# Optimization experiments

Measured on AMD Instinct MI355X. Metric: run time of the kernel, lower is better.

The kernel has to match this reference:

```python
import jax, jax.numpy as jnp
import numpy as np

B, T, F, U = 128, 512, 128, 512  # batch, time, features, GRU units


def _gru(x, W, Urec, bi, br, return_sequences):
    """Keras GRU (reset_after=True, recurrent_activation=sigmoid, activation=relu).
    x: (B, T, F_in); W: (F_in, 3U); Urec: (U, 3U); bi, br: (3U,). Gate order: z, r, h.
    """
    b = x.shape[0]
    u = Urec.shape[0]
    # precompute all input-projected gates: (T, B, 3U)
    gx = jnp.transpose(jnp.einsum('bti,ig->btg', x, W) + bi, (1, 0, 2))
    h0 = jnp.zeros((b, u), x.dtype)

    def step(h, g):
        rec = h @ Urec + br                      # (B, 3U)
        xz, xr, xh = jnp.split(g, 3, axis=-1)
        rz, rr, rh = jnp.split(rec, 3, axis=-1)
        z = jax.nn.sigmoid(xz + rz)              # update gate
        r = jax.nn.sigmoid(xr + rr)              # reset gate
        hh = jax.nn.relu(xh + r * rh)            # candidate (relu activation)
        h_new = z * h + (1.0 - z) * hh
        return h_new, h_new

    h_last, hs = jax.lax.scan(step, h0, gx)
    if return_sequences:
        return jnp.transpose(hs, (1, 0, 2))      # (B, T, U)
    return h_last                                # (B, U)


def setup_inputs() -> dict:
    key = jax.random.key(0)
    ks = jax.random.split(key, 8)
    s_in1 = 1.0 / np.sqrt(F)
    s_rec = 1.0 / np.sqrt(U)
    return {
        'x':   jax.random.normal(ks[0], (B, T, F), jnp.float32),
        'W1':  jax.random.normal(ks[1], (F, 3 * U), jnp.float32) * s_in1,
        'U1':  jax.random.normal(ks[2], (U, 3 * U), jnp.float32) * s_rec,
        'bi1': jnp.zeros((3 * U,), jnp.float32),
        'br1': jnp.zeros((3 * U,), jnp.float32),
        'W2':  jax.random.normal(ks[3], (U, 3 * U), jnp.float32) * s_rec,
        'U2':  jax.random.normal(ks[4], (U, 3 * U), jnp.float32) * s_rec,
        'bi2': jnp.zeros((3 * U,), jnp.float32),
        'br2': jnp.zeros((3 * U,), jnp.float32),
        'Wd':  jax.random.normal(ks[5], (U, 1), jnp.float32) * s_rec,
        'bd':  jnp.zeros((1,), jnp.float32),
    }


def reference(x, W1, U1, bi1, br1, W2, U2, bi2, br2, Wd, bd):
    h_seq = _gru(x, W1, U1, bi1, br1, True)      # (B, T, U)
    h = _gru(h_seq, W2, U2, bi2, br2, False)     # (B, U)
    return h @ Wd + bd
```

## Files before the change

### kernel.cpp

```cpp
#include <hip/hip_runtime.h>
#include <cstdint>
#include <cstddef>

#define B_  128
#define T_  512
#define F_  128
#define U_  512
#define G3  1536
#define BU  (B_ * U_)

#define NGRP 8
#define MB   16
#define GN   32
#define UC   16

typedef __attribute__((ext_vector_type(8))) _Float16 half8;
typedef __attribute__((ext_vector_type(4))) float    f32x4;

union HU16 { _Float16 h; unsigned short us; };

__device__ __forceinline__ float sigmoidf_(float x) {
    return 1.0f / (1.0f + __expf(-x));
}

__device__ __forceinline__ void vm_drain() {
    asm volatile("s_waitcnt vmcnt(0)" ::: "memory");
}

__device__ __forceinline__ void load_h16(const _Float16* aptr, half8* f) {
    asm volatile(
        "global_load_dwordx4 %0, %16, off offset:0 sc0 sc1\n\t"
        "global_load_dwordx4 %1, %16, off offset:64 sc0 sc1\n\t"
        "global_load_dwordx4 %2, %16, off offset:128 sc0 sc1\n\t"
        "global_load_dwordx4 %3, %16, off offset:192 sc0 sc1\n\t"
        "global_load_dwordx4 %4, %16, off offset:256 sc0 sc1\n\t"
        "global_load_dwordx4 %5, %16, off offset:320 sc0 sc1\n\t"
        "global_load_dwordx4 %6, %16, off offset:384 sc0 sc1\n\t"
        "global_load_dwordx4 %7, %16, off offset:448 sc0 sc1\n\t"
        "global_load_dwordx4 %8, %16, off offset:512 sc0 sc1\n\t"
        "global_load_dwordx4 %9, %16, off offset:576 sc0 sc1\n\t"
        "global_load_dwordx4 %10, %16, off offset:640 sc0 sc1\n\t"
        "global_load_dwordx4 %11, %16, off offset:704 sc0 sc1\n\t"
        "global_load_dwordx4 %12, %16, off offset:768 sc0 sc1\n\t"
        "global_load_dwordx4 %13, %16, off offset:832 sc0 sc1\n\t"
        "global_load_dwordx4 %14, %16, off offset:896 sc0 sc1\n\t"
        "global_load_dwordx4 %15, %16, off offset:960 sc0 sc1"
        : "=&v"(f[0]), "=&v"(f[1]), "=&v"(f[2]), "=&v"(f[3]),
          "=&v"(f[4]), "=&v"(f[5]), "=&v"(f[6]), "=&v"(f[7]),
          "=&v"(f[8]), "=&v"(f[9]), "=&v"(f[10]), "=&v"(f[11]),
          "=&v"(f[12]), "=&v"(f[13]), "=&v"(f[14]), "=&v"(f[15])
        : "v"((uint64_t)(uintptr_t)aptr)
        : "memory");
}

__device__ __forceinline__ void wait_h16(half8* f) {
    asm volatile(
        "s_waitcnt vmcnt(0)"
        : "+v"(f[0]), "+v"(f[1]), "+v"(f[2]), "+v"(f[3]),
          "+v"(f[4]), "+v"(f[5]), "+v"(f[6]), "+v"(f[7]),
          "+v"(f[8]), "+v"(f[9]), "+v"(f[10]), "+v"(f[11]),
          "+v"(f[12]), "+v"(f[13]), "+v"(f[14]), "+v"(f[15])
        :
        : "memory");
}

__device__ __forceinline__ void store_h4(_Float16* addr, unsigned v0, unsigned v1,
                                         unsigned v2, unsigned v3) {
    asm volatile(
        "global_store_short %0, %1, off sc0 sc1\n\t"
        "global_store_short %0, %2, off offset:1024 sc0 sc1\n\t"
        "global_store_short %0, %3, off offset:2048 sc0 sc1\n\t"
        "global_store_short %0, %4, off offset:3072 sc0 sc1"
        :: "v"((uint64_t)(uintptr_t)addr), "v"(v0), "v"(v1), "v"(v2), "v"(v3)
        : "memory");
}

__device__ __forceinline__ void flag_set(unsigned* p, unsigned val) {
    asm volatile("global_store_dword %0, %1, off sc0 sc1"
                 :: "v"((uint64_t)(uintptr_t)p), "v"(val) : "memory");
}

__device__ __forceinline__ unsigned flag_get(const unsigned* p) {
    unsigned v;
    asm volatile("global_load_dword %0, %1, off sc0 sc1\n\ts_waitcnt vmcnt(0)"
                 : "=v"(v) : "v"((uint64_t)(uintptr_t)p) : "memory");
    return v;
}

__device__ __forceinline__ void poll_flags(const unsigned* base, int lane, unsigned tgt) {
    const unsigned* p = base + (lane & 31);
    while (!__all((int)(flag_get(p) >= tgt))) {}
}

__global__ void cast_init_kernel(const float* __restrict__ x,
                                 _Float16* __restrict__ xh,
                                 _Float16* __restrict__ h1pub,
                                 _Float16* __restrict__ h2pub,
                                 unsigned int* __restrict__ gbar) {
    size_t i      = (size_t)blockIdx.x * blockDim.x + threadIdx.x;
    size_t stride = (size_t)gridDim.x * blockDim.x;
    for (size_t idx = i; idx < (size_t)B_ * T_ * F_; idx += stride)
        xh[idx] = (_Float16)x[idx];
    for (size_t idx = i; idx < (size_t)3 * BU; idx += stride)
        h1pub[idx] = (_Float16)0.f;
    for (size_t idx = i; idx < (size_t)2 * BU; idx += stride)
        h2pub[idx] = (_Float16)0.f;
    if (blockIdx.x == 0)
        for (int idx = threadIdx.x; idx < 2048; idx += blockDim.x)
            gbar[idx] = 0u;
}

__global__ void transpose_cast_kernel(const float* __restrict__ in,
                                      _Float16* __restrict__ out, int K) {
    __shared__ float tile[32][33];
    int n0 = blockIdx.x * 32;
    int k0 = blockIdx.y * 32;
    int tx = threadIdx.x, ty = threadIdx.y;
#pragma unroll
    for (int i = 0; i < 4; ++i)
        tile[ty + i * 8][tx] = in[(size_t)(k0 + ty + i * 8) * G3 + (n0 + tx)];
    __syncthreads();
#pragma unroll
    for (int i = 0; i < 4; ++i)
        out[(size_t)(n0 + ty + i * 8) * K + (k0 + tx)] =
            (_Float16)tile[tx][ty + i * 8];
}

__global__ __launch_bounds__(256) void gemm_gx1_kernel(
    const _Float16* __restrict__ xh,
    const _Float16* __restrict__ w1t,
    _Float16* __restrict__ gx1) {
    int bx = blockIdx.x;
    int mb = bx / 12, nb = bx % 12;
    int wave = threadIdx.x >> 6, lane = threadIdx.x & 63;
    int wm = wave >> 1, wn = wave & 1;
    int am = lane & 15, aq = lane >> 4;

    half8 af[2][4];
#pragma unroll
    for (int mt = 0; mt < 2; ++mt) {
        int mo = mb * 64 + wm * 32 + mt * 16 + am;
        int b = mo & 127, t = mo >> 7;
        const _Float16* ap = xh + ((size_t)b * T_ + t) * F_ + aq * 8;
#pragma unroll
        for (int kc = 0; kc < 4; ++kc)
            af[mt][kc] = *(const half8*)(ap + kc * 32);
    }

#pragma unroll
    for (int nt = 0; nt < 4; ++nt) {
        int n0 = nb * 128 + wn * 64 + nt * 16;
        f32x4 acc0 = {0.f, 0.f, 0.f, 0.f};
        f32x4 acc1 = {0.f, 0.f, 0.f, 0.f};
#pragma unroll
        for (int kc = 0; kc < 4; ++kc) {
            half8 bf = *(const half8*)(w1t + (size_t)(n0 + am) * F_ + kc * 32 + aq * 8);
            acc0 = __builtin_amdgcn_mfma_f32_16x16x32_f16(af[0][kc], bf, acc0, 0, 0, 0);
            acc1 = __builtin_amdgcn_mfma_f32_16x16x32_f16(af[1][kc], bf, acc1, 0, 0, 0);
        }
        int col = lane & 15, rb = (lane >> 4) * 4;
        int mbase0 = mb * 64 + wm * 32 + 0 * 16;
        int mbase1 = mb * 64 + wm * 32 + 1 * 16;
#pragma unroll
        for (int i = 0; i < 4; ++i) {
            gx1[(size_t)(mbase0 + rb + i) * G3 + n0 + col] = (_Float16)acc0[i];
            gx1[(size_t)(mbase1 + rb + i) * G3 + n0 + col] = (_Float16)acc1[i];
        }
    }
}

__global__ __launch_bounds__(192, 1) void gru_persist_kernel(
    const _Float16* __restrict__ gx1,
    const _Float16* __restrict__ u1t,
    const _Float16* __restrict__ w2t,
    const _Float16* __restrict__ u2t,
    const float* __restrict__ bi1, const float* __restrict__ br1,
    const float* __restrict__ bi2, const float* __restrict__ br2,
    _Float16* __restrict__ h1pub,
    _Float16* __restrict__ h2pub,
    float* __restrict__ h2fin,
    unsigned int* __restrict__ gbar) {
    __shared__ float scr[2 * 3 * 16 * 17];

    const int tid  = threadIdx.x;
    const int bx   = blockIdx.x;
    const int grp  = bx & 7;
    const int jj   = bx >> 3;
    const int wave = tid >> 6, lane = tid & 63;
    const int row0 = grp * MB;
    const int u0   = jj * UC;

    unsigned* flag1 = gbar + 512  + (size_t)grp * 32;
    unsigned* flag2 = gbar + 1024 + (size_t)grp * 32;
    unsigned* myflag1 = flag1 + jj;
    unsigned* myflag2 = flag2 + jj;

    const int col = lane & 15;
    const int rb4 = (lane >> 4) * 4;
    const int aq  = lane >> 4;
    const size_t a_elem = (size_t)(row0 + col) * U_ + aq * 8;
    const int u = u0 + col;

    const _Float16* wsrc = (wave == 0) ? u1t : (wave == 1) ? w2t : u2t;
    half8 bfr[3][16];
#pragma unroll
    for (int g = 0; g < 3; ++g)
#pragma unroll
        for (int kc = 0; kc < 16; ++kc)
            bfr[g][kc] = *(const half8*)(
                wsrc + (size_t)(g * U_ + u0 + col) * U_ + kc * 32 + aq * 8);

    float zb = 0.f, rb_ = 0.f, hbi = 0.f, hbr = 0.f;
    _Float16 pgz[4], pgr[4], pgh[4];
    if (wave == 0) {
        zb  = bi1[u] + br1[u];
        rb_ = bi1[U_ + u] + br1[U_ + u];
        hbi = bi1[2 * U_ + u];
        hbr = br1[2 * U_ + u];
        const _Float16* g0 = gx1 + ((size_t)0 * B_ + row0 + rb4) * G3;
#pragma unroll
        for (int i = 0; i < 4; ++i) {
            pgz[i] = g0[(size_t)i * G3 + u];
            pgr[i] = g0[(size_t)i * G3 + U_ + u];
            pgh[i] = g0[(size_t)i * G3 + 2 * U_ + u];
        }
    } else if (wave == 2) {
        zb  = bi2[u] + br2[u];
        rb_ = bi2[U_ + u] + br2[U_ + u];
        hbi = bi2[2 * U_ + u];
        hbr = br2[2 * U_ + u];
    }

    float st[4] = {0.f, 0.f, 0.f, 0.f};

    int wr3 = 0, rd3 = 2;
    for (int r = 0; r <= T_ + 1; ++r) {
        if (wave == 0) {
            if (r < T_) {
                poll_flags(flag1, lane, (unsigned)r);
                _Float16 ngz[4], ngr[4], ngh[4];
                bool pf = (r + 1 < T_);
                if (pf) {
                    const _Float16* g = gx1 + ((size_t)(r + 1) * B_ + row0 + rb4) * G3;
#pragma unroll
                    for (int i = 0; i < 4; ++i) {
                        ngz[i] = g[(size_t)i * G3 + u];
                        ngr[i] = g[(size_t)i * G3 + U_ + u];
                        ngh[i] = g[(size_t)i * G3 + 2 * U_ + u];
                    }
                }
                half8 f[16];
                load_h16(h1pub + (size_t)rd3 * BU + a_elem, f);
                wait_h16(f);
                f32x4 a0 = {0.f, 0.f, 0.f, 0.f};
                f32x4 a1 = {0.f, 0.f, 0.f, 0.f};
                f32x4 a2 = {0.f, 0.f, 0.f, 0.f};
#pragma unroll
                for (int kc = 0; kc < 16; ++kc) {
                    a0 = __builtin_amdgcn_mfma_f32_16x16x32_f16(f[kc], bfr[0][kc], a0, 0, 0, 0);
                    a1 = __builtin_amdgcn_mfma_f32_16x16x32_f16(f[kc], bfr[1][kc], a1, 0, 0, 0);
                    a2 = __builtin_amdgcn_mfma_f32_16x16x32_f16(f[kc], bfr[2][kc], a2, 0, 0, 0);
                }
                unsigned pv[4];
#pragma unroll
                for (int i = 0; i < 4; ++i) {
                    float z  = sigmoidf_((float)pgz[i] + a0[i] + zb);
                    float rg = sigmoidf_((float)pgr[i] + a1[i] + rb_);
                    float hh = fmaxf(0.f, (float)pgh[i] + hbi + rg * (a2[i] + hbr));
                    st[i] = z * st[i] + (1.f - z) * hh;
                    HU16 c; c.h = (_Float16)st[i]; pv[i] = c.us;
                }
                _Float16* dst = h1pub + (size_t)wr3 * BU +
                                (size_t)(row0 + rb4) * U_ + u;
                store_h4(dst, pv[0], pv[1], pv[2], pv[3]);
                vm_drain();
                if (lane == 0) flag_set(myflag1, (unsigned)(r + 1));
                if (pf) {
#pragma unroll
                    for (int i = 0; i < 4; ++i) {
                        pgz[i] = ngz[i]; pgr[i] = ngr[i]; pgh[i] = ngh[i];
                    }
                }
            }
        } else if (wave == 1) {
            if (r >= 1 && r <= T_) {
                poll_flags(flag1, lane, (unsigned)r);
                half8 f[16];
                load_h16(h1pub + (size_t)rd3 * BU + a_elem, f);
                wait_h16(f);
                f32x4 a0 = {0.f, 0.f, 0.f, 0.f};
                f32x4 a1 = {0.f, 0.f, 0.f, 0.f};
                f32x4 a2 = {0.f, 0.f, 0.f, 0.f};
#pragma unroll
                for (int kc = 0; kc < 16; ++kc) {
                    a0 = __builtin_amdgcn_mfma_f32_16x16x32_f16(f[kc], bfr[0][kc], a0, 0, 0, 0);
                    a1 = __builtin_amdgcn_mfma_f32_16x16x32_f16(f[kc], bfr[1][kc], a1, 0, 0, 0);
                    a2 = __builtin_amdgcn_mfma_f32_16x16x32_f16(f[kc], bfr[2][kc], a2, 0, 0, 0);
                }
                float* sp = scr + (size_t)(r & 1) * 3 * 272;
#pragma unroll
                for (int i = 0; i < 4; ++i) {
                    sp[0 * 272 + (rb4 + i) * 17 + col] = a0[i];
                    sp[1 * 272 + (rb4 + i) * 17 + col] = a1[i];
                    sp[2 * 272 + (rb4 + i) * 17 + col] = a2[i];
                }
            }
        } else {
            if (r >= 2) {
                int s = r - 2;
                poll_flags(flag2, lane, (unsigned)(r - 2));
                half8 f[16];
                load_h16(h2pub + (size_t)((r - 1) & 1) * BU + a_elem, f);
                wait_h16(f);
                f32x4 a0 = {0.f, 0.f, 0.f, 0.f};
                f32x4 a1 = {0.f, 0.f, 0.f, 0.f};
                f32x4 a2 = {0.f, 0.f, 0.f, 0.f};
#pragma unroll
                for (int kc = 0; kc < 16; ++kc) {
                    a0 = __builtin_amdgcn_mfma_f32_16x16x32_f16(f[kc], bfr[0][kc], a0, 0, 0, 0);
                    a1 = __builtin_amdgcn_mfma_f32_16x16x32_f16(f[kc], bfr[1][kc], a1, 0, 0, 0);
                    a2 = __builtin_amdgcn_mfma_f32_16x16x32_f16(f[kc], bfr[2][kc], a2, 0, 0, 0);
                }
                const float* sp = scr + (size_t)((r - 1) & 1) * 3 * 272;
                unsigned pv[4];
#pragma unroll
                for (int i = 0; i < 4; ++i) {
                    int ro = (rb4 + i) * 17 + col;
                    float z  = sigmoidf_(sp[0 * 272 + ro] + a0[i] + zb);
                    float rg = sigmoidf_(sp[1 * 272 + ro] + a1[i] + rb_);
                    float hh = fmaxf(0.f, sp[2 * 272 + ro] + hbi + rg * (a2[i] + hbr));
                    st[i] = z * st[i] + (1.f - z) * hh;
                    HU16 c; c.h = (_Float16)st[i]; pv[i] = c.us;
                }
                _Float16* dst = h2pub + (size_t)(s & 1) * BU +
                                (size_t)(row0 + rb4) * U_ + u;
                store_h4(dst, pv[0], pv[1], pv[2], pv[3]);
                vm_drain();
                if (lane == 0) flag_set(myflag2, (unsigned)(s + 1));
                if (s == T_ - 1) {
#pragma unroll
                    for (int i = 0; i < 4; ++i)
                        h2fin[(size_t)(row0 + rb4 + i) * U_ + u] = st[i];
                }
            }
        }
        __syncthreads();
        wr3 = (wr3 == 2) ? 0 : wr3 + 1;
        rd3 = (rd3 == 2) ? 0 : rd3 + 1;
    }
}

__global__ void head_kernel(const float* __restrict__ h2fin,
                            const float* __restrict__ Wd,
                            const float* __restrict__ bd,
                            float* __restrict__ out) {
    int b = blockIdx.x;
    int lane = threadIdx.x;
    float s = 0.f;
#pragma unroll
    for (int u = lane; u < U_; u += 64)
        s += h2fin[(size_t)b * U_ + u] * Wd[u];
#pragma unroll
    for (int off = 32; off > 0; off >>= 1)
        s += __shfl_down(s, off, 64);
    if (lane == 0) out[b] = s + bd[0];
}

extern "C" void kernel_launch(void* const* d_in, const int* in_sizes, int n_in,
                              void* d_out, int out_size, void* d_ws, size_t ws_size,
                              hipStream_t stream) {
    (void)in_sizes; (void)n_in; (void)out_size; (void)ws_size;

    const float* x   = (const float*)d_in[0];
    const float* W1  = (const float*)d_in[1];
    const float* U1  = (const float*)d_in[2];
    const float* bi1 = (const float*)d_in[3];
    const float* br1 = (const float*)d_in[4];
    const float* W2  = (const float*)d_in[5];
    const float* U2  = (const float*)d_in[6];
    const float* bi2 = (const float*)d_in[7];
    const float* br2 = (const float*)d_in[8];
    const float* Wd  = (const float*)d_in[9];
    const float* bd  = (const float*)d_in[10];

    char* w = (char*)d_ws;
    constexpr size_t OFF_XH   = 0;
    constexpr size_t OFF_W1T  = OFF_XH  + (size_t)B_ * T_ * F_ * 2;
    constexpr size_t OFF_U1T  = OFF_W1T + (size_t)G3 * F_ * 2;
    constexpr size_t OFF_W2T  = OFF_U1T + (size_t)G3 * U_ * 2;
    constexpr size_t OFF_U2T  = OFF_W2T + (size_t)G3 * U_ * 2;
    constexpr size_t OFF_GX1  = OFF_U2T + (size_t)G3 * U_ * 2;
    constexpr size_t OFF_H1P  = OFF_GX1 + (size_t)T_ * B_ * G3 * 2;
    constexpr size_t OFF_H2P  = OFF_H1P + (size_t)3 * BU * 2;
    constexpr size_t OFF_H2F  = OFF_H2P + (size_t)2 * BU * 2;
    constexpr size_t OFF_BAR  = OFF_H2F + (size_t)BU * 4;

    _Float16* xh   = (_Float16*)(w + OFF_XH);
    _Float16* w1t  = (_Float16*)(w + OFF_W1T);
    _Float16* u1t  = (_Float16*)(w + OFF_U1T);
    _Float16* w2t  = (_Float16*)(w + OFF_W2T);
    _Float16* u2t  = (_Float16*)(w + OFF_U2T);
    _Float16* gx1  = (_Float16*)(w + OFF_GX1);
    _Float16* h1p  = (_Float16*)(w + OFF_H1P);
    _Float16* h2p  = (_Float16*)(w + OFF_H2P);
    float*    h2f  = (float*)   (w + OFF_H2F);
    unsigned int* gbar = (unsigned int*)(w + OFF_BAR);

    cast_init_kernel<<<1024, 256, 0, stream>>>(x, xh, h1p, h2p, gbar);

    dim3 tb(32, 8);
    transpose_cast_kernel<<<dim3(48, 4),  tb, 0, stream>>>(W1, w1t, F_);
    transpose_cast_kernel<<<dim3(48, 16), tb, 0, stream>>>(U1, u1t, U_);
    transpose_cast_kernel<<<dim3(48, 16), tb, 0, stream>>>(W2, w2t, U_);
    transpose_cast_kernel<<<dim3(48, 16), tb, 0, stream>>>(U2, u2t, U_);

    gemm_gx1_kernel<<<12288, 256, 0, stream>>>(xh, w1t, gx1);

    gru_persist_kernel<<<256, 192, 0, stream>>>(gx1, u1t, w2t, u2t,
                                                bi1, br1, bi2, br2,
                                                h1p, h2p, h2f, gbar);

    head_kernel<<<128, 64, 0, stream>>>(h2f, Wd, bd, (float*)d_out);
}
```

Before: 1.937 ms.

## Replace per-step block barrier with LDS progress flags and share h1 via LDS

Removes the __syncthreads lockstep between the three role waves, replacing it with per-wave progress counters in shared memory so each wave can run ahead within bounded slack. Wave 0 also copies its loaded h1 fragments into a double-buffered LDS area, so wave 1 reads them from LDS instead of polling global flags and reloading from global memory. The aim is to decouple the layer-2 input projection from the layer-1 recurrence critical path and cut global traffic. This adds spin-waiting on LDS and relies on the memory-ordering of relaxed atomics plus lgkmcnt drains being correct.

```diff
diff --git a/kernel.cpp b/kernel.cpp
--- a/kernel.cpp
+++ b/kernel.cpp
@@ -25,6 +25,10 @@
 
 __device__ __forceinline__ void vm_drain() {
     asm volatile("s_waitcnt vmcnt(0)" ::: "memory");
+}
+
+__device__ __forceinline__ void lgkm_drain() {
+    asm volatile("s_waitcnt lgkmcnt(0)" ::: "memory");
 }
 
 __device__ __forceinline__ void load_h16(const _Float16* aptr, half8* f) {
@@ -92,6 +96,13 @@
     while (!__all((int)(flag_get(p) >= tgt))) {}
 }
 
+__device__ __forceinline__ int lds_ld(const int* p) {
+    return __hip_atomic_load(p, __ATOMIC_RELAXED, __HIP_MEMORY_SCOPE_WORKGROUP);
+}
+__device__ __forceinline__ void lds_st(int* p, int v) {
+    __hip_atomic_store(p, v, __ATOMIC_RELAXED, __HIP_MEMORY_SCOPE_WORKGROUP);
+}
+
 __global__ void cast_init_kernel(const float* __restrict__ x,
                                  _Float16* __restrict__ xh,
                                  _Float16* __restrict__ h1pub,
@@ -180,7 +191,9 @@
     _Float16* __restrict__ h2pub,
     float* __restrict__ h2fin,
     unsigned int* __restrict__ gbar) {
-    __shared__ float scr[2 * 3 * 16 * 17];
+    __shared__ _Float16 acp[2 * 16 * 512];
+    __shared__ float    scr[2 * 3 * 272];
+    __shared__ int      prog[16];
 
     const int tid  = threadIdx.x;
     const int bx   = blockIdx.x;
@@ -210,143 +223,179 @@
             bfr[g][kc] = *(const half8*)(
                 wsrc + (size_t)(g * U_ + u0 + col) * U_ + kc * 32 + aq * 8);
 
-    float zb = 0.f, rb_ = 0.f, hbi = 0.f, hbr = 0.f;
-    _Float16 pgz[4], pgr[4], pgh[4];
+    if (tid < 16) prog[tid] = 0;
+    __syncthreads();
+
     if (wave == 0) {
-        zb  = bi1[u] + br1[u];
-        rb_ = bi1[U_ + u] + br1[U_ + u];
-        hbi = bi1[2 * U_ + u];
-        hbr = br1[2 * U_ + u];
-        const _Float16* g0 = gx1 + ((size_t)0 * B_ + row0 + rb4) * G3;
-#pragma unroll
-        for (int i = 0; i < 4; ++i) {
-            pgz[i] = g0[(size_t)i * G3 + u];
-            pgr[i] = g0[(size_t)i * G3 + U_ + u];
-            pgh[i] = g0[(size_t)i * G3 + 2 * U_ + u];
-        }
-    } else if (wave == 2) {
-        zb  = bi2[u] + br2[u];
-        rb_ = bi2[U_ + u] + br2[U_ + u];
-        hbi = bi2[2 * U_ + u];
-        hbr = br2[2 * U_ + u];
-    }
-
-    float st[4] = {0.f, 0.f, 0.f, 0.f};
-
-    int wr3 = 0, rd3 = 2;
-    for (int r = 0; r <= T_ + 1; ++r) {
-        if (wave == 0) {
-            if (r < T_) {
-                poll_flags(flag1, lane, (unsigned)r);
-                _Float16 ngz[4], ngr[4], ngh[4];
-                bool pf = (r + 1 < T_);
-                if (pf) {
-                    const _Float16* g = gx1 + ((size_t)(r + 1) * B_ + row0 + rb4) * G3;
-#pragma unroll
-                    for (int i = 0; i < 4; ++i) {
-                        ngz[i] = g[(size_t)i * G3 + u];
-                        ngr[i] = g[(size_t)i * G3 + U_ + u];
-                        ngh[i] = g[(size_t)i * G3 + 2 * U_ + u];
-                    }
+        const float zb  = bi1[u] + br1[u];
+        const float rb_ = bi1[U_ + u] + br1[U_ + u];
+        const float hbi = bi1[2 * U_ + u];
+        const float hbr = br1[2 * U_ + u];
+        _Float16 pgz[4], pgr[4], pgh[4];
+        {
+            const _Float16* g0 = gx1 + ((size_t)0 * B_ + row0 + rb4) * G3;
+#pragma unroll
+            for (int i = 0; i < 4; ++i) {
+                pgz[i] = g0[(size_t)i * G3 + u];
+                pgr[i] = g0[(size_t)i * G3 + U_ + u];
+                pgh[i] = g0[(size_t)i * G3 + 2 * U_ + u];
+            }
+        }
+        float st[4] = {0.f, 0.f, 0.f, 0.f};
+
+        for (int r = 0; r < T_; ++r) {
+            _Float16 ngz[4], ngr[4], ngh[4];
+            bool pf = (r + 1 < T_);
+            if (pf) {
+                const _Float16* g = gx1 + ((size_t)(r + 1) * B_ + row0 + rb4) * G3;
+#pragma unroll
+                for (int i = 0; i < 4; ++i) {
+                    ngz[i] = g[(size_t)i * G3 + u];
+                    ngr[i] = g[(size_t)i * G3 + U_ + u];
+                    ngh[i] = g[(size_t)i * G3 + 2 * U_ + u];
                 }
-                half8 f[16];
-                load_h16(h1pub + (size_t)rd3 * BU + a_elem, f);
-                wait_h16(f);
-                f32x4 a0 = {0.f, 0.f, 0.f, 0.f};
-                f32x4 a1 = {0.f, 0.f, 0.f, 0.f};
-                f32x4 a2 = {0.f, 0.f, 0.f, 0.f};
-#pragma unroll
-                for (int kc = 0; kc < 16; ++kc) {
-                    a0 = __builtin_amdgcn_mfma_f32_16x16x32_f16(f[kc], bfr[0][kc], a0, 0, 0, 0);
-                    a1 = __builtin_amdgcn_mfma_f32_16x16x32_f16(f[kc], bfr[1][kc], a1, 0, 0, 0);
-                    a2 = __builtin_amdgcn_mfma_f32_16x16x32_f16(f[kc], bfr[2][kc], a2, 0, 0, 0);
+            }
+            poll_flags(flag1, lane, (unsigned)r);
+            half8 f[16];
+            load_h16(h1pub + (size_t)((r + 2) % 3) * BU + a_elem, f);
+            wait_h16(f);
+            f32x4 a0 = {0.f, 0.f, 0.f, 0.f};
+            f32x4 a1 = {0.f, 0.f, 0.f, 0.f};
+            f32x4 a2 = {0.f, 0.f, 0.f, 0.f};
+#pragma unroll
+            for (int kc = 0; kc < 16; ++kc) {
+                a0 = __builtin_amdgcn_mfma_f32_16x16x32_f16(f[kc], bfr[0][kc], a0, 0, 0, 0);
+                a1 = __builtin_amdgcn_mfma_f32_16x16x32_f16(f[kc], bfr[1][kc], a1, 0, 0, 0);
+                a2 = __builtin_amdgcn_mfma_f32_16x16x32_f16(f[kc], bfr[2][kc], a2, 0, 0, 0);
+            }
+            unsigned pv[4];
+#pragma unroll
+            for (int i = 0; i < 4; ++i) {
+                float z  = sigmoidf_((float)pgz[i] + a0[i] + zb);
+                float rg = sigmoidf_((float)pgr[i] + a1[i] + rb_);
+                float hh = fmaxf(0.f, (float)pgh[i] + hbi + rg * (a2[i] + hbr));
+                st[i] = z * st[i] + (1.f - z) * hh;
+                HU16 c; c.h = (_Float16)st[i]; pv[i] = c.us;
+            }
+            _Float16* dst = h1pub + (size_t)(r % 3) * BU +
+                            (size_t)(row0 + rb4) * U_ + u;
+            store_h4(dst, pv[0], pv[1], pv[2], pv[3]);
+            vm_drain();
+            if (lane == 0) flag_set(myflag1, (unsigned)(r + 1));
+            if (pf) {
+#pragma unroll
+                for (int i = 0; i < 4; ++i) {
+                    pgz[i] = ngz[i]; pgr[i] = ngr[i]; pgh[i] = ngh[i];
                 }
-                unsigned pv[4];
-#pragma unroll
-                for (int i = 0; i < 4; ++i) {
-                    float z  = sigmoidf_((float)pgz[i] + a0[i] + zb);
-                    float rg = sigmoidf_((float)pgr[i] + a1[i] + rb_);
-                    float hh = fmaxf(0.f, (float)pgh[i] + hbi + rg * (a2[i] + hbr));
-                    st[i] = z * st[i] + (1.f - z) * hh;
-                    HU16 c; c.h = (_Float16)st[i]; pv[i] = c.us;
-                }
-                _Float16* dst = h1pub + (size_t)wr3 * BU +
-                                (size_t)(row0 + rb4) * U_ + u;
-                store_h4(dst, pv[0], pv[1], pv[2], pv[3]);
-                vm_drain();
-                if (lane == 0) flag_set(myflag1, (unsigned)(r + 1));
-                if (pf) {
-#pragma unroll
-                    for (int i = 0; i < 4; ++i) {
-                        pgz[i] = ngz[i]; pgr[i] = ngr[i]; pgh[i] = ngh[i];
-                    }
-                }
-            }
-        } else if (wave == 1) {
-            if (r >= 1 && r <= T_) {
-                poll_flags(flag1, lane, (unsigned)r);
-                half8 f[16];
-                load_h16(h1pub + (size_t)rd3 * BU + a_elem, f);
-                wait_h16(f);
-                f32x4 a0 = {0.f, 0.f, 0.f, 0.f};
-                f32x4 a1 = {0.f, 0.f, 0.f, 0.f};
-                f32x4 a2 = {0.f, 0.f, 0.f, 0.f};
-#pragma unroll
-                for (int kc = 0; kc < 16; ++kc) {
-                    a0 = __builtin_amdgcn_mfma_f32_16x16x32_f16(f[kc], bfr[0][kc], a0, 0, 0, 0);
-                    a1 = __builtin_amdgcn_mfma_f32_16x16x32_f16(f[kc], bfr[1][kc], a1, 0, 0, 0);
-                    a2 = __builtin_amdgcn_mfma_f32_16x16x32_f16(f[kc], bfr[2][kc], a2, 0, 0, 0);
-                }
-                float* sp = scr + (size_t)(r & 1) * 3 * 272;
-#pragma unroll
-                for (int i = 0; i < 4; ++i) {
-                    sp[0 * 272 + (rb4 + i) * 17 + col] = a0[i];
-                    sp[1 * 272 + (rb4 + i) * 17 + col] = a1[i];
-                    sp[2 * 272 + (rb4 + i) * 17 + col] = a2[i];
-                }
-            }
-        } else {
-            if (r >= 2) {
-                int s = r - 2;
-                poll_flags(flag2, lane, (unsigned)(r - 2));
-                half8 f[16];
-                load_h16(h2pub + (size_t)((r - 1) & 1) * BU + a_elem, f);
-                wait_h16(f);
-                f32x4 a0 = {0.f, 0.f, 0.f, 0.f};
-                f32x4 a1 = {0.f, 0.f, 0.f, 0.f};
-                f32x4 a2 = {0.f, 0.f, 0.f, 0.f};
-#pragma unroll
-                for (int kc = 0; kc < 16; ++kc) {
-                    a0 = __builtin_amdgcn_mfma_f32_16x16x32_f16(f[kc], bfr[0][kc], a0, 0, 0, 0);
-                    a1 = __builtin_amdgcn_mfma_f32_16x16x32_f16(f[kc], bfr[1][kc], a1, 0, 0, 0);
-                    a2 = __builtin_amdgcn_mfma_f32_16x16x32_f16(f[kc], bfr[2][kc], a2, 0, 0, 0);
-                }
-                const float* sp = scr + (size_t)((r - 1) & 1) * 3 * 272;
-                unsigned pv[4];
-#pragma unroll
-                for (int i = 0; i < 4; ++i) {
-                    int ro = (rb4 + i) * 17 + col;
-                    float z  = sigmoidf_(sp[0 * 272 + ro] + a0[i] + zb);
-                    float rg = sigmoidf_(sp[1 * 272 + ro] + a1[i] + rb_);
-                    float hh = fmaxf(0.f, sp[2 * 272 + ro] + hbi + rg * (a2[i] + hbr));
-                    st[i] = z * st[i] + (1.f - z) * hh;
-                    HU16 c; c.h = (_Float16)st[i]; pv[i] = c.us;
-                }
-                _Float16* dst = h2pub + (size_t)(s & 1) * BU +
-                                (size_t)(row0 + rb4) * U_ + u;
-                store_h4(dst, pv[0], pv[1], pv[2], pv[3]);
-                vm_drain();
-                if (lane == 0) flag_set(myflag2, (unsigned)(s + 1));
-                if (s == T_ - 1) {
-#pragma unroll
-                    for (int i = 0; i < 4; ++i)
-                        h2fin[(size_t)(row0 + rb4 + i) * U_ + u] = st[i];
-                }
-            }
-        }
-        __syncthreads();
-        wr3 = (wr3 == 2) ? 0 : wr3 + 1;
-        rd3 = (rd3 == 2) ? 0 : rd3 + 1;
+            }
+            while (lds_ld(&prog[1]) < r - 2) {}
+            _Float16* ab = acp + (size_t)(r & 1) * (16 * 512);
+#pragma unroll
+            for (int kc = 0; kc < 16; ++kc)
+                *(half8*)(ab + kc * 512 + lane * 8) = f[kc];
+            lgkm_drain();
+            lds_st(&prog[0], r + 1);
+        }
+    } else if (wave == 1) {
+        for (int r = 1; r < T_; ++r) {
+            while (lds_ld(&prog[0]) < r + 1) {}
+            while (lds_ld(&prog[2]) < r - 2) {}
+            const _Float16* ab = acp + (size_t)(r & 1) * (16 * 512);
+            half8 f[16];
+#pragma unroll
+            for (int kc = 0; kc < 16; ++kc)
+                f[kc] = *(const half8*)(ab + kc * 512 + lane * 8);
+            f32x4 a0 = {0.f, 0.f, 0.f, 0.f};
+            f32x4 a1 = {0.f, 0.f, 0.f, 0.f};
+            f32x4 a2 = {0.f, 0.f, 0.f, 0.f};
+#pragma unroll
+            for (int kc = 0; kc < 16; ++kc) {
+                a0 = __builtin_amdgcn_mfma_f32_16x16x32_f16(f[kc], bfr[0][kc], a0, 0, 0, 0);
+                a1 = __builtin_amdgcn_mfma_f32_16x16x32_f16(f[kc], bfr[1][kc], a1, 0, 0, 0);
+                a2 = __builtin_amdgcn_mfma_f32_16x16x32_f16(f[kc], bfr[2][kc], a2, 0, 0, 0);
+            }
+            float* sp = scr + (size_t)((r - 1) & 1) * 3 * 272;
+#pragma unroll
+            for (int i = 0; i < 4; ++i) {
+                sp[0 * 272 + (rb4 + i) * 17 + col] = a0[i];
+                sp[1 * 272 + (rb4 + i) * 17 + col] = a1[i];
+                sp[2 * 272 + (rb4 + i) * 17 + col] = a2[i];
+            }
+            lgkm_drain();
+            lds_st(&prog[1], r);
+        }
+        {
+            const int r = T_;
+            while (lds_ld(&prog[2]) < r - 2) {}
+            poll_flags(flag1, lane, (unsigned)T_);
+            half8 f[16];
+            load_h16(h1pub + (size_t)((T_ - 1) % 3) * BU + a_elem, f);
+            wait_h16(f);
+            f32x4 a0 = {0.f, 0.f, 0.f, 0.f};
+            f32x4 a1 = {0.f, 0.f, 0.f, 0.f};
+            f32x4 a2 = {0.f, 0.f, 0.f, 0.f};
+#pragma unroll
+            for (int kc = 0; kc < 16; ++kc) {
+                a0 = __builtin_amdgcn_mfma_f32_16x16x32_f16(f[kc], bfr[0][kc], a0, 0, 0, 0);
+                a1 = __builtin_amdgcn_mfma_f32_16x16x32_f16(f[kc], bfr[1][kc], a1, 0, 0, 0);
+                a2 = __builtin_amdgcn_mfma_f32_16x16x32_f16(f[kc], bfr[2][kc], a2, 0, 0, 0);
+            }
+            float* sp = scr + (size_t)((r - 1) & 1) * 3 * 272;
+#pragma unroll
+            for (int i = 0; i < 4; ++i) {
+                sp[0 * 272 + (rb4 + i) * 17 + col] = a0[i];
+                sp[1 * 272 + (rb4 + i) * 17 + col] = a1[i];
+                sp[2 * 272 + (rb4 + i) * 17 + col] = a2[i];
+            }
+            lgkm_drain();
+            lds_st(&prog[1], r);
+        }
+    } else {
+        const float zb  = bi2[u] + br2[u];
+        const float rb_ = bi2[U_ + u] + br2[U_ + u];
+        const float hbi = bi2[2 * U_ + u];
+        const float hbr = br2[2 * U_ + u];
+        float st[4] = {0.f, 0.f, 0.f, 0.f};
+
+        for (int s = 0; s < T_; ++s) {
+            while (lds_ld(&prog[1]) < s + 1) {}
+            poll_flags(flag2, lane, (unsigned)s);
+            half8 f[16];
+            load_h16(h2pub + (size_t)((s + 1) & 1) * BU + a_elem, f);
+            wait_h16(f);
+            f32x4 a0 = {0.f, 0.f, 0.f, 0.f};
+            f32x4 a1 = {0.f, 0.f, 0.f, 0.f};
+            f32x4 a2 = {0.f, 0.f, 0.f, 0.f};
+#pragma unroll
+            for (int kc = 0; kc < 16; ++kc) {
+                a0 = __builtin_amdgcn_mfma_f32_16x16x32_f16(f[kc], bfr[0][kc], a0, 0, 0, 0);
+                a1 = __builtin_amdgcn_mfma_f32_16x16x32_f16(f[kc], bfr[1][kc], a1, 0, 0, 0);
+                a2 = __builtin_amdgcn_mfma_f32_16x16x32_f16(f[kc], bfr[2][kc], a2, 0, 0, 0);
+            }
+            const float* sp = scr + (size_t)(s & 1) * 3 * 272;
+            unsigned pv[4];
+#pragma unroll
+            for (int i = 0; i < 4; ++i) {
+                int ro = (rb4 + i) * 17 + col;
+                float z  = sigmoidf_(sp[0 * 272 + ro] + a0[i] + zb);
+                float rg = sigmoidf_(sp[1 * 272 + ro] + a1[i] + rb_);
+                float hh = fmaxf(0.f, sp[2 * 272 + ro] + hbi + rg * (a2[i] + hbr));
+                st[i] = z * st[i] + (1.f - z) * hh;
+                HU16 c; c.h = (_Float16)st[i]; pv[i] = c.us;
+            }
+            _Float16* dst = h2pub + (size_t)(s & 1) * BU +
+                            (size_t)(row0 + rb4) * U_ + u;
+            store_h4(dst, pv[0], pv[1], pv[2], pv[3]);
+            vm_drain();
+            if (lane == 0) flag_set(myflag2, (unsigned)(s + 1));
+            lgkm_drain();
+            lds_st(&prog[2], s + 1);
+            if (s == T_ - 1) {
+#pragma unroll
+                for (int i = 0; i < 4; ++i)
+                    h2fin[(size_t)(row0 + rb4 + i) * U_ + u] = st[i];
+            }
+        }
     }
 }
 
```

New measurement: 1.950 ms. Within noise of the previous version (+0.7%).
